# Optimization experiments

Measured on AMD Instinct MI355X. Metric: run time of the kernel, lower is better.

Reference implementation:

```python
import jax, jax.numpy as jnp
import numpy as np

B, T, F = 256, 512, 256
H, C = 1024, 128


def setup_inputs() -> dict:
    key = jax.random.key(0)
    ks = jax.random.split(key, 12)
    s = 0.05
    return {
        "y": jax.random.normal(ks[0], (B, T, F), jnp.float32),
        "W_ih1": jax.random.normal(ks[1], (4 * H, F), jnp.float32) * s,
        "W_hh1": jax.random.normal(ks[2], (4 * H, H), jnp.float32) * s,
        "b_ih1": jax.random.normal(ks[3], (4 * H,), jnp.float32) * s,
        "b_hh1": jax.random.normal(ks[4], (4 * H,), jnp.float32) * s,
        "W_ih2": jax.random.normal(ks[5], (4 * H, H), jnp.float32) * s,
        "W_hh2": jax.random.normal(ks[6], (4 * H, H), jnp.float32) * s,
        "b_ih2": jax.random.normal(ks[7], (4 * H,), jnp.float32) * s,
        "b_hh2": jax.random.normal(ks[8], (4 * H,), jnp.float32) * s,
        "W_out": jax.random.normal(ks[9], (C, H), jnp.float32) * s,
        "b_out": jax.random.normal(ks[10], (C,), jnp.float32) * s,
    }


def _lstm_cell(x, h, c, W_ih, W_hh, b_ih, b_hh):
    # PyTorch LSTMCell: gates ordered i, f, g, o
    gates = x @ W_ih.T + b_ih + h @ W_hh.T + b_hh
    i, f, g, o = jnp.split(gates, 4, axis=-1)
    i, f, o = jax.nn.sigmoid(i), jax.nn.sigmoid(f), jax.nn.sigmoid(o)
    g = jnp.tanh(g)
    c_new = f * c + i * g
    h_new = o * jnp.tanh(c_new)
    return h_new, c_new


def reference(y, W_ih1, W_hh1, b_ih1, b_hh1, W_ih2, W_hh2, b_ih2, b_hh2, W_out, b_out):
    n = y.shape[0]
    z = jnp.zeros((n, H), jnp.float32)

    def step(carry, x_t):
        h1, c1, h2, c2 = carry
        h1, c1 = _lstm_cell(x_t, h1, c1, W_ih1, W_hh1, b_ih1, b_hh1)
        h2, c2 = _lstm_cell(h1, h2, c2, W_ih2, W_hh2, b_ih2, b_hh2)
        h2 = jnp.tanh(h2)  # note: tanh'd h2 is also the recurrent state, as in source
        out = jax.nn.relu(h2 @ W_out.T + b_out)
        return (h1, c1, h2, c2), out

    xs = jnp.transpose(y, (1, 0, 2))  # [T, B, F]
    _, outs = jax.lax.scan(step, (z, z, z, z), xs)
    # return_sequences=False -> last timestep output [B, C]
    return outs[-1]
```

## Files before the change

### kernel.cpp

```cpp
#include <hip/hip_runtime.h>
#include <hip/hip_bf16.h>

#define Bb 256
#define Tt 512
#define Ff 256
#define Hh 1024
#define Cc 128
#define NBLK 256
#define NTHR 512

typedef __bf16 bf16;
typedef bf16 bf16x8 __attribute__((ext_vector_type(8)));
typedef float f32x4 __attribute__((ext_vector_type(4)));

#define MFMA(a, b, c) __builtin_amdgcn_mfma_f32_16x16x32_bf16(a, b, c, 0, 0, 0)

struct SMem {
    bf16x8 w[2 * 64 * 64];
    float scratch[32 * 129];
    float bias[32];
    bf16 hstage[8 * 256];
};

__device__ __forceinline__ float fsig(float x) {
    x = fminf(30.f, fmaxf(-30.f, x));
    return __builtin_amdgcn_rcpf(1.f + __expf(-x));
}
__device__ __forceinline__ float ftanh(float x) {
    x = fminf(15.f, fmaxf(-15.f, x));
    float e = __expf(2.f * x);
    return (e - 1.f) * __builtin_amdgcn_rcpf(e + 1.f);
}

#define STX4_SC1(p, v) \
    asm volatile("global_store_dwordx4 %0, %1, off sc1" :: "v"(p), "v"(v) : "memory")
#define LDX4_PLAIN(dst, base, OFF) \
    asm volatile("global_load_dwordx4 %0, %1, off offset:" #OFF : "=v"(dst) : "v"(base))

#define ISSUE_CHUNK(B0, B1, P0, P1) do { \
    LDX4_PLAIN(B0[0], (P0), 0);   LDX4_PLAIN(B0[1], (P0), 64);  LDX4_PLAIN(B0[2], (P0), 128); LDX4_PLAIN(B0[3], (P0), 192); \
    LDX4_PLAIN(B0[4], (P0), 256); LDX4_PLAIN(B0[5], (P0), 320); LDX4_PLAIN(B0[6], (P0), 384); LDX4_PLAIN(B0[7], (P0), 448); \
    LDX4_PLAIN(B1[0], (P1), 0);   LDX4_PLAIN(B1[1], (P1), 64);  LDX4_PLAIN(B1[2], (P1), 128); LDX4_PLAIN(B1[3], (P1), 192); \
    LDX4_PLAIN(B1[4], (P1), 256); LDX4_PLAIN(B1[5], (P1), 320); LDX4_PLAIN(B1[6], (P1), 384); LDX4_PLAIN(B1[7], (P1), 448); \
} while (0)

#define WAITV(N, B0, B1) \
    asm volatile("s_waitcnt vmcnt(" #N ")" : \
        "+v"(B0[0]), "+v"(B0[1]), "+v"(B0[2]), "+v"(B0[3]), \
        "+v"(B0[4]), "+v"(B0[5]), "+v"(B0[6]), "+v"(B0[7]), \
        "+v"(B1[0]), "+v"(B1[1]), "+v"(B1[2]), "+v"(B1[3]), \
        "+v"(B1[4]), "+v"(B1[5]), "+v"(B1[6]), "+v"(B1[7]) :: "memory")

#define MFMA8(ABASE, B0, B1) do { \
    _Pragma("unroll") \
    for (int _i = 0; _i < 8; ++_i) { \
        bf16x8 _a0 = wA0[((ABASE) + _i) * 64 + lane]; \
        bf16x8 _a1 = wA1[((ABASE) + _i) * 64 + lane]; \
        bf16x8 _b0 = __builtin_bit_cast(bf16x8, B0[_i]); \
        bf16x8 _b1 = __builtin_bit_cast(bf16x8, B1[_i]); \
        acc00 = MFMA(_a0, _b0, acc00); acc10 = MFMA(_a1, _b0, acc10); \
        acc01 = MFMA(_a0, _b1, acc01); acc11 = MFMA(_a1, _b1, acc11); \
    } \
} while (0)

__device__ __forceinline__ void mm32(const bf16x8* __restrict__ wA0, const bf16x8* __restrict__ wA1,
                                     int abase, const bf16* p0, const bf16* p1, int lane,
                                     f32x4& acc00, f32x4& acc01, f32x4& acc10, f32x4& acc11)
{
    f32x4 bx0[8], bx1[8], by0[8], by1[8];
    asm volatile("s_waitcnt vmcnt(0)" ::: "memory");
    ISSUE_CHUNK(bx0, bx1, p0, p1);
    ISSUE_CHUNK(by0, by1, p0 + 256, p1 + 256);
    WAITV(16, bx0, bx1);
    MFMA8(abase + 0, bx0, bx1);
    ISSUE_CHUNK(bx0, bx1, p0 + 512, p1 + 512);
    WAITV(16, by0, by1);
    MFMA8(abase + 8, by0, by1);
    ISSUE_CHUNK(by0, by1, p0 + 768, p1 + 768);
    WAITV(16, bx0, bx1);
    MFMA8(abase + 16, bx0, bx1);
    WAITV(0, by0, by1);
    MFMA8(abase + 24, by0, by1);
}

__device__ __forceinline__ void epilogue(SMem& sm, f32x4 acc00, f32x4 acc01, f32x4 acc10, f32x4 acc11,
                                         float creg[4], bf16* hdst, int hu0, bool extra_tanh) {
    const int tid = threadIdx.x;
    const int lane = tid & 63, wv = tid >> 6, quad = lane >> 4, l15 = lane & 15;
    const int colb = (wv & 3) * 32;
    #pragma unroll
    for (int ph = 0; ph < 2; ++ph) {
        if ((wv >> 2) == ph) {
            #pragma unroll
            for (int r = 0; r < 4; ++r) {
                sm.scratch[(quad * 4 + r) * 129 + colb + l15]           = acc00[r];
                sm.scratch[(quad * 4 + r) * 129 + colb + 16 + l15]      = acc01[r];
                sm.scratch[(16 + quad * 4 + r) * 129 + colb + l15]      = acc10[r];
                sm.scratch[(16 + quad * 4 + r) * 129 + colb + 16 + l15] = acc11[r];
            }
        }
        __syncthreads();
        #pragma unroll
        for (int pi = 0; pi < 2; ++pi) {
            int idx = pi * NTHR + tid;
            int bl = idx & 127, hu = idx >> 7;
            float gi = sm.scratch[hu * 129 + bl]        + sm.bias[hu];
            float gf = sm.scratch[(8 + hu) * 129 + bl]  + sm.bias[8 + hu];
            float gg = sm.scratch[(16 + hu) * 129 + bl] + sm.bias[16 + hu];
            float go = sm.scratch[(24 + hu) * 129 + bl] + sm.bias[24 + hu];
            float iv = fsig(gi), fv = fsig(gf), gv = ftanh(gg), ov = fsig(go);
            float c = fv * creg[ph * 2 + pi] + iv * gv;
            creg[ph * 2 + pi] = c;
            float h = ov * ftanh(c);
            if (extra_tanh) h = ftanh(h);
            sm.hstage[hu * 256 + (bl + 128 * ph)] = (bf16)h;
        }
        __syncthreads();
    }
    if (tid < 256) {
        bf16x8 v;
        #pragma unroll
        for (int e = 0; e < 8; ++e) v[e] = sm.hstage[e * 256 + tid];
        bf16* p = hdst + (size_t)tid * Hh + hu0;
        f32x4 pv = __builtin_bit_cast(f32x4, v);
        STX4_SC1(p, pv);
    }
}

__global__ void __launch_bounds__(NTHR, 2)
lstm_kernel(const float* __restrict__ y,
            const float* __restrict__ Wih1, const float* __restrict__ Whh1,
            const float* __restrict__ bih1, const float* __restrict__ bhh1,
            const float* __restrict__ Wih2, const float* __restrict__ Whh2,
            const float* __restrict__ bih2, const float* __restrict__ bhh2,
            const float* __restrict__ Wout, const float* __restrict__ bout,
            float* __restrict__ out,
            bf16* __restrict__ h1b0, bf16* __restrict__ h1b1,
            bf16* __restrict__ h2b0, bf16* __restrict__ h2b1,
            char* __restrict__ ctl)
{
    __shared__ SMem sm;
    const int tid = threadIdx.x;
    const int bid = blockIdx.x;
    const bool isL2 = bid >= 128;
    const int hu0 = (bid & 127) * 8;
    const int KI = isL2 ? 64 : 40;
    const int lane = tid & 63;
    const int wv = tid >> 6;
    const int quad = lane >> 4;
    const int l15 = lane & 15;

    unsigned* boot   = (unsigned*)ctl;
    unsigned* arrive = (unsigned*)(ctl + 2048);

    if (tid < 32) {
        int gate = tid >> 3, j = tid & 7;
        int grow = gate * Hh + hu0 + j;
        sm.bias[tid] = isL2 ? (bih2[grow] + bhh2[grow]) : (bih1[grow] + bhh1[grow]);
    }
    for (int slot = tid; slot < 2 * KI * 64; slot += NTHR) {
        int mt = slot / (KI * 64);
        int ki = (slot / 64) % KI;
        int ln = slot & 63;
        int row = mt * 16 + (ln & 15);
        int k = ki * 32 + (ln >> 4) * 8;
        int gate = row >> 3, j = row & 7;
        int grow = gate * Hh + hu0 + j;
        const float* src;
        if (!isL2) src = (k < Ff) ? (Wih1 + (size_t)grow * Ff + k) : (Whh1 + (size_t)grow * Hh + (k - Ff));
        else       src = (k < Hh) ? (Wih2 + (size_t)grow * Hh + k) : (Whh2 + (size_t)grow * Hh + (k - Hh));
        bf16x8 fr;
        #pragma unroll
        for (int e = 0; e < 8; ++e) fr[e] = (bf16)src[e];
        sm.w[slot] = fr;
    }
    float creg[4] = {0.f, 0.f, 0.f, 0.f};
    __syncthreads();

    if (tid == 0)
        __hip_atomic_store(&boot[bid], 1u, __ATOMIC_RELAXED, __HIP_MEMORY_SCOPE_AGENT);
    if (tid < 64) {
        for (;;) {
            int ok = 1;
            #pragma unroll
            for (int j = 0; j < 4; ++j)
                ok &= (__hip_atomic_load(&boot[tid * 4 + j], __ATOMIC_RELAXED,
                                         __HIP_MEMORY_SCOPE_AGENT) >= 1u);
            if (__all(ok)) break;
            __builtin_amdgcn_s_sleep(4);
        }
    }
    __syncthreads();

    const int nb0 = wv * 32 + l15;
    const bf16x8* wA0 = sm.w;
    const bf16x8* wA1 = sm.w + KI * 64;

    for (int s = 0; s <= Tt; ++s) {
        const int t = isL2 ? (s - 1) : s;
        const bool active = isL2 ? (s >= 1) : (s < Tt);
        f32x4 acc00 = {0,0,0,0}, acc01 = {0,0,0,0}, acc10 = {0,0,0,0}, acc11 = {0,0,0,0};

        if (!isL2 && active) {
            const f32x4* x0v = (const f32x4*)(y + ((size_t)nb0 * Tt + t) * Ff) + quad * 2;
            const f32x4* x1v = x0v + (size_t)16 * Tt * (Ff / 4);
            #pragma unroll
            for (int ki = 0; ki < 8; ++ki) {
                bf16x8 a0 = wA0[ki * 64 + lane];
                bf16x8 a1 = wA1[ki * 64 + lane];
                f32x4 u0 = x0v[ki * 8], u1 = x0v[ki * 8 + 1];
                f32x4 w0 = x1v[ki * 8], w1 = x1v[ki * 8 + 1];
                bf16x8 b0, b1;
                #pragma unroll
                for (int e = 0; e < 4; ++e) {
                    b0[e] = (bf16)u0[e]; b0[4 + e] = (bf16)u1[e];
                    b1[e] = (bf16)w0[e]; b1[4 + e] = (bf16)w1[e];
                }
                acc00 = MFMA(a0, b0, acc00); acc10 = MFMA(a1, b0, acc10);
                acc01 = MFMA(a0, b1, acc01); acc11 = MFMA(a1, b1, acc11);
            }
        }

        if (s >= 1) {
            const unsigned e = (unsigned)s;
            if (tid < 64) {
                for (;;) {
                    int ok = 1;
                    #pragma unroll
                    for (int j = 0; j < 4; ++j)
                        ok &= (__hip_atomic_load(&arrive[tid * 4 + j], __ATOMIC_RELAXED,
                                                 __HIP_MEMORY_SCOPE_AGENT) >= e);
                    if (__all(ok)) break;
                    __builtin_amdgcn_s_sleep(2);
                }
                __builtin_amdgcn_fence(__ATOMIC_ACQUIRE, "agent");
            }
            __syncthreads();
        }

        if (active) {
            const bf16* h1rd = ((s - 1) & 1) ? h1b1 : h1b0;
            if (!isL2) {
                if (t > 0) {
                    const bf16* p0 = h1rd + (size_t)nb0 * Hh + quad * 8;
                    mm32(wA0, wA1, 8, p0, p0 + 16 * Hh, lane, acc00, acc01, acc10, acc11);
                }
                epilogue(sm, acc00, acc01, acc10, acc11, creg, (t & 1) ? h1b1 : h1b0, hu0, false);
            } else {
                const bf16* p0 = h1rd + (size_t)nb0 * Hh + quad * 8;
                mm32(wA0, wA1, 0, p0, p0 + 16 * Hh, lane, acc00, acc01, acc10, acc11);
                if (t > 0) {
                    const bf16* h2rd = (s & 1) ? h2b1 : h2b0;
                    const bf16* q0 = h2rd + (size_t)nb0 * Hh + quad * 8;
                    mm32(wA0, wA1, 32, q0, q0 + 16 * Hh, lane, acc00, acc01, acc10, acc11);
                }
                epilogue(sm, acc00, acc01, acc10, acc11, creg, (t & 1) ? h2b1 : h2b0, hu0, true);
            }
        }

        __syncthreads();
        if (tid == 0)
            __hip_atomic_store(&arrive[bid], (unsigned)(s + 1), __ATOMIC_RELAXED,
                               __HIP_MEMORY_SCOPE_AGENT);
    }

    {
        const unsigned e = (unsigned)(Tt + 1);
        if (tid < 64) {
            for (;;) {
                int ok = 1;
                #pragma unroll
                for (int j = 0; j < 4; ++j)
                    ok &= (__hip_atomic_load(&arrive[tid * 4 + j], __ATOMIC_RELAXED,
                                             __HIP_MEMORY_SCOPE_AGENT) >= e);
                if (__all(ok)) break;
                __builtin_amdgcn_s_sleep(2);
            }
            __builtin_amdgcn_fence(__ATOMIC_ACQUIRE, "agent");
        }
        __syncthreads();
    }

    if (bid < 16) {
        const int bb = bid * 16 + l15;
        const float* ap = Wout + (size_t)(wv * 16 + l15) * Hh + quad * 8;
        const bf16* bp = h2b1 + (size_t)bb * Hh + quad * 8;
        f32x4 acc = {0,0,0,0};
        #pragma unroll 4
        for (int ki = 0; ki < 32; ++ki) {
            bf16x8 a;
            #pragma unroll
            for (int e = 0; e < 8; ++e) a[e] = (bf16)ap[ki * 32 + e];
            bf16x8 b = *(const bf16x8*)(bp + ki * 32);
            acc = MFMA(a, b, acc);
        }
        #pragma unroll
        for (int r = 0; r < 4; ++r) {
            int orow = wv * 16 + quad * 4 + r;
            float v = acc[r] + bout[orow];
            out[(size_t)bb * Cc + orow] = fmaxf(v, 0.f);
        }
    }
}

extern "C" void kernel_launch(void* const* d_in, const int* in_sizes, int n_in,
                              void* d_out, int out_size, void* d_ws, size_t ws_size,
                              hipStream_t stream) {
    const float* y    = (const float*)d_in[0];
    const float* Wih1 = (const float*)d_in[1];
    const float* Whh1 = (const float*)d_in[2];
    const float* bih1 = (const float*)d_in[3];
    const float* bhh1 = (const float*)d_in[4];
    const float* Wih2 = (const float*)d_in[5];
    const float* Whh2 = (const float*)d_in[6];
    const float* bih2 = (const float*)d_in[7];
    const float* bhh2 = (const float*)d_in[8];
    const float* Wout = (const float*)d_in[9];
    const float* bout = (const float*)d_in[10];
    float* out = (float*)d_out;

    char* wsteal = (char*)d_in[2] + ((size_t)4 * Hh * Hh * sizeof(float) - 4 * 524288);
    bf16* h1b0 = (bf16*)(wsteal);
    bf16* h1b1 = (bf16*)(wsteal + 1 * 524288);
    bf16* h2b0 = (bf16*)(wsteal + 2 * 524288);
    bf16* h2b1 = (bf16*)(wsteal + 3 * 524288);

    char* ctl = (char*)d_ws;
    hipMemsetAsync(ctl, 0, 32768, stream);

    void* args[] = { &y, &Wih1, &Whh1, &bih1, &bhh1, &Wih2, &Whh2, &bih2, &bhh2,
                     &Wout, &bout, &out, &h1b0, &h1b1, &h2b0, &h2b1, &ctl };
    hipLaunchCooperativeKernel((void*)lstm_kernel, dim3(NBLK), dim3(NTHR), args, 0, stream);
}
```

Measured before the change: 19.18 ms.

## Interleave gate rows so LSTM epilogue runs in registers; rotate K chunks per block

Weight rows are reordered so each MFMA output quad holds the i,f,g,o gates of one hidden unit for one batch row. The cell update can then be computed directly from accumulator registers, with biases held in registers. This removes the shared-memory scratch transpose and most of the block barriers in the per-step epilogue. The K-chunk load order is also rotated per block to spread simultaneous reads of the shared h buffers, and layer 2's two matmuls are merged into one pipelined 64-chunk loop. The trade-off is more address arithmetic and a different summation order, which slightly changes the rounding of the results.

```diff
diff --git a/kernel.cpp b/kernel.cpp
--- a/kernel.cpp
+++ b/kernel.cpp
@@ -17,9 +17,7 @@
 
 struct SMem {
     bf16x8 w[2 * 64 * 64];
-    float scratch[32 * 129];
-    float bias[32];
-    bf16 hstage[8 * 256];
+    bf16 hstage[256 * 8];
 };
 
 __device__ __forceinline__ float fsig(float x) {
@@ -63,64 +61,90 @@
     } \
 } while (0)
 
+__device__ __forceinline__ const bf16* phsel(int idx, const bf16* p, const bf16* q) {
+    return ((idx < 4) ? p : q) + (idx & 3) * 256;
+}
+
 __device__ __forceinline__ void mm32(const bf16x8* __restrict__ wA0, const bf16x8* __restrict__ wA1,
-                                     int abase, const bf16* p0, const bf16* p1, int lane,
+                                     int abase, const bf16* p0, const bf16* p1, int lane, int rot,
                                      f32x4& acc00, f32x4& acc01, f32x4& acc10, f32x4& acc11)
 {
     f32x4 bx0[8], bx1[8], by0[8], by1[8];
+    const int c0 = rot & 3, c1 = (rot + 1) & 3, c2 = (rot + 2) & 3, c3 = (rot + 3) & 3;
+    const bf16* a0 = p0 + c0 * 256; const bf16* a1 = p1 + c0 * 256;
+    const bf16* b0 = p0 + c1 * 256; const bf16* b1 = p1 + c1 * 256;
+    const bf16* d0 = p0 + c2 * 256; const bf16* d1 = p1 + c2 * 256;
+    const bf16* e0 = p0 + c3 * 256; const bf16* e1 = p1 + c3 * 256;
     asm volatile("s_waitcnt vmcnt(0)" ::: "memory");
-    ISSUE_CHUNK(bx0, bx1, p0, p1);
-    ISSUE_CHUNK(by0, by1, p0 + 256, p1 + 256);
+    ISSUE_CHUNK(bx0, bx1, a0, a1);
+    ISSUE_CHUNK(by0, by1, b0, b1);
     WAITV(16, bx0, bx1);
-    MFMA8(abase + 0, bx0, bx1);
-    ISSUE_CHUNK(bx0, bx1, p0 + 512, p1 + 512);
+    MFMA8(abase + c0 * 8, bx0, bx1);
+    ISSUE_CHUNK(bx0, bx1, d0, d1);
     WAITV(16, by0, by1);
-    MFMA8(abase + 8, by0, by1);
-    ISSUE_CHUNK(by0, by1, p0 + 768, p1 + 768);
+    MFMA8(abase + c1 * 8, by0, by1);
+    ISSUE_CHUNK(by0, by1, e0, e1);
     WAITV(16, bx0, bx1);
-    MFMA8(abase + 16, bx0, bx1);
+    MFMA8(abase + c2 * 8, bx0, bx1);
     WAITV(0, by0, by1);
-    MFMA8(abase + 24, by0, by1);
+    MFMA8(abase + c3 * 8, by0, by1);
+}
+
+__device__ __forceinline__ void mm64(const bf16x8* __restrict__ wA0, const bf16x8* __restrict__ wA1,
+                                     const bf16* p0, const bf16* p1,
+                                     const bf16* q0, const bf16* q1, int lane, int rot,
+                                     f32x4& acc00, f32x4& acc01, f32x4& acc10, f32x4& acc11)
+{
+    f32x4 bx0[8], bx1[8], by0[8], by1[8];
+    const int i0 = rot & 7, i1 = (rot + 1) & 7, i2 = (rot + 2) & 7, i3 = (rot + 3) & 7;
+    const int i4 = (rot + 4) & 7, i5 = (rot + 5) & 7, i6 = (rot + 6) & 7, i7 = (rot + 7) & 7;
+    asm volatile("s_waitcnt vmcnt(0)" ::: "memory");
+    { const bf16* u0 = phsel(i0, p0, q0); const bf16* u1 = phsel(i0, p1, q1); ISSUE_CHUNK(bx0, bx1, u0, u1); }
+    { const bf16* u0 = phsel(i1, p0, q0); const bf16* u1 = phsel(i1, p1, q1); ISSUE_CHUNK(by0, by1, u0, u1); }
+    WAITV(16, bx0, bx1); MFMA8(i0 * 8, bx0, bx1);
+    { const bf16* u0 = phsel(i2, p0, q0); const bf16* u1 = phsel(i2, p1, q1); ISSUE_CHUNK(bx0, bx1, u0, u1); }
+    WAITV(16, by0, by1); MFMA8(i1 * 8, by0, by1);
+    { const bf16* u0 = phsel(i3, p0, q0); const bf16* u1 = phsel(i3, p1, q1); ISSUE_CHUNK(by0, by1, u0, u1); }
+    WAITV(16, bx0, bx1); MFMA8(i2 * 8, bx0, bx1);
+    { const bf16* u0 = phsel(i4, p0, q0); const bf16* u1 = phsel(i4, p1, q1); ISSUE_CHUNK(bx0, bx1, u0, u1); }
+    WAITV(16, by0, by1); MFMA8(i3 * 8, by0, by1);
+    { const bf16* u0 = phsel(i5, p0, q0); const bf16* u1 = phsel(i5, p1, q1); ISSUE_CHUNK(by0, by1, u0, u1); }
+    WAITV(16, bx0, bx1); MFMA8(i4 * 8, bx0, bx1);
+    { const bf16* u0 = phsel(i6, p0, q0); const bf16* u1 = phsel(i6, p1, q1); ISSUE_CHUNK(bx0, bx1, u0, u1); }
+    WAITV(16, by0, by1); MFMA8(i5 * 8, by0, by1);
+    { const bf16* u0 = phsel(i7, p0, q0); const bf16* u1 = phsel(i7, p1, q1); ISSUE_CHUNK(by0, by1, u0, u1); }
+    WAITV(16, bx0, bx1); MFMA8(i6 * 8, bx0, bx1);
+    WAITV(0, by0, by1); MFMA8(i7 * 8, by0, by1);
+}
+
+__device__ __forceinline__ float lstm_cell(const f32x4& acc, const f32x4& bq, float& c, bool extra_tanh) {
+    float iv = fsig(acc[0] + bq[0]);
+    float fv = fsig(acc[1] + bq[1]);
+    float gv = ftanh(acc[2] + bq[2]);
+    float ov = fsig(acc[3] + bq[3]);
+    float cn = fv * c + iv * gv;
+    c = cn;
+    float h = ov * ftanh(cn);
+    return extra_tanh ? ftanh(h) : h;
 }
 
 __device__ __forceinline__ void epilogue(SMem& sm, f32x4 acc00, f32x4 acc01, f32x4 acc10, f32x4 acc11,
+                                         const f32x4& bq0, const f32x4& bq1,
                                          float creg[4], bf16* hdst, int hu0, bool extra_tanh) {
     const int tid = threadIdx.x;
     const int lane = tid & 63, wv = tid >> 6, quad = lane >> 4, l15 = lane & 15;
-    const int colb = (wv & 3) * 32;
-    #pragma unroll
-    for (int ph = 0; ph < 2; ++ph) {
-        if ((wv >> 2) == ph) {
-            #pragma unroll
-            for (int r = 0; r < 4; ++r) {
-                sm.scratch[(quad * 4 + r) * 129 + colb + l15]           = acc00[r];
-                sm.scratch[(quad * 4 + r) * 129 + colb + 16 + l15]      = acc01[r];
-                sm.scratch[(16 + quad * 4 + r) * 129 + colb + l15]      = acc10[r];
-                sm.scratch[(16 + quad * 4 + r) * 129 + colb + 16 + l15] = acc11[r];
-            }
-        }
-        __syncthreads();
-        #pragma unroll
-        for (int pi = 0; pi < 2; ++pi) {
-            int idx = pi * NTHR + tid;
-            int bl = idx & 127, hu = idx >> 7;
-            float gi = sm.scratch[hu * 129 + bl]        + sm.bias[hu];
-            float gf = sm.scratch[(8 + hu) * 129 + bl]  + sm.bias[8 + hu];
-            float gg = sm.scratch[(16 + hu) * 129 + bl] + sm.bias[16 + hu];
-            float go = sm.scratch[(24 + hu) * 129 + bl] + sm.bias[24 + hu];
-            float iv = fsig(gi), fv = fsig(gf), gv = ftanh(gg), ov = fsig(go);
-            float c = fv * creg[ph * 2 + pi] + iv * gv;
-            creg[ph * 2 + pi] = c;
-            float h = ov * ftanh(c);
-            if (extra_tanh) h = ftanh(h);
-            sm.hstage[hu * 256 + (bl + 128 * ph)] = (bf16)h;
-        }
-        __syncthreads();
-    }
+    const int b0 = wv * 32 + l15;
+    float h00 = lstm_cell(acc00, bq0, creg[0], extra_tanh);
+    float h01 = lstm_cell(acc01, bq0, creg[1], extra_tanh);
+    float h10 = lstm_cell(acc10, bq1, creg[2], extra_tanh);
+    float h11 = lstm_cell(acc11, bq1, creg[3], extra_tanh);
+    sm.hstage[b0 * 8 + quad]            = (bf16)h00;
+    sm.hstage[(b0 + 16) * 8 + quad]     = (bf16)h01;
+    sm.hstage[b0 * 8 + 4 + quad]        = (bf16)h10;
+    sm.hstage[(b0 + 16) * 8 + 4 + quad] = (bf16)h11;
+    __syncthreads();
     if (tid < 256) {
-        bf16x8 v;
-        #pragma unroll
-        for (int e = 0; e < 8; ++e) v[e] = sm.hstage[e * 256 + tid];
+        bf16x8 v = *(const bf16x8*)&sm.hstage[tid * 8];
         bf16* p = hdst + (size_t)tid * Hh + hu0;
         f32x4 pv = __builtin_bit_cast(f32x4, v);
         STX4_SC1(p, pv);
@@ -149,22 +173,28 @@
     const int wv = tid >> 6;
     const int quad = lane >> 4;
     const int l15 = lane & 15;
+    const int rot4 = bid & 3;
+    const int rot8 = bid & 7;
 
     unsigned* boot   = (unsigned*)ctl;
     unsigned* arrive = (unsigned*)(ctl + 2048);
 
-    if (tid < 32) {
-        int gate = tid >> 3, j = tid & 7;
-        int grow = gate * Hh + hu0 + j;
-        sm.bias[tid] = isL2 ? (bih2[grow] + bhh2[grow]) : (bih1[grow] + bhh1[grow]);
+    f32x4 bq0, bq1;
+    #pragma unroll
+    for (int r = 0; r < 4; ++r) {
+        int g0 = r * Hh + hu0 + quad;
+        int g1 = r * Hh + hu0 + 4 + quad;
+        bq0[r] = isL2 ? (bih2[g0] + bhh2[g0]) : (bih1[g0] + bhh1[g0]);
+        bq1[r] = isL2 ? (bih2[g1] + bhh2[g1]) : (bih1[g1] + bhh1[g1]);
     }
     for (int slot = tid; slot < 2 * KI * 64; slot += NTHR) {
         int mt = slot / (KI * 64);
         int ki = (slot / 64) % KI;
         int ln = slot & 63;
-        int row = mt * 16 + (ln & 15);
+        int local = ln & 15;
         int k = ki * 32 + (ln >> 4) * 8;
-        int gate = row >> 3, j = row & 7;
+        int gate = local & 3;
+        int j = mt * 4 + (local >> 2);
         int grow = gate * Hh + hu0 + j;
         const float* src;
         if (!isL2) src = (k < Ff) ? (Wih1 + (size_t)grow * Ff + k) : (Whh1 + (size_t)grow * Hh + (k - Ff));
@@ -243,18 +273,22 @@
             if (!isL2) {
                 if (t > 0) {
                     const bf16* p0 = h1rd + (size_t)nb0 * Hh + quad * 8;
-                    mm32(wA0, wA1, 8, p0, p0 + 16 * Hh, lane, acc00, acc01, acc10, acc11);
+                    mm32(wA0, wA1, 8, p0, p0 + 16 * Hh, lane, rot4, acc00, acc01, acc10, acc11);
                 }
-                epilogue(sm, acc00, acc01, acc10, acc11, creg, (t & 1) ? h1b1 : h1b0, hu0, false);
+                epilogue(sm, acc00, acc01, acc10, acc11, bq0, bq1, creg,
+                         (t & 1) ? h1b1 : h1b0, hu0, false);
             } else {
                 const bf16* p0 = h1rd + (size_t)nb0 * Hh + quad * 8;
-                mm32(wA0, wA1, 0, p0, p0 + 16 * Hh, lane, acc00, acc01, acc10, acc11);
                 if (t > 0) {
                     const bf16* h2rd = (s & 1) ? h2b1 : h2b0;
                     const bf16* q0 = h2rd + (size_t)nb0 * Hh + quad * 8;
-                    mm32(wA0, wA1, 32, q0, q0 + 16 * Hh, lane, acc00, acc01, acc10, acc11);
+                    mm64(wA0, wA1, p0, p0 + 16 * Hh, q0, q0 + 16 * Hh, lane, rot8,
+                         acc00, acc01, acc10, acc11);
+                } else {
+                    mm32(wA0, wA1, 0, p0, p0 + 16 * Hh, lane, rot4, acc00, acc01, acc10, acc11);
                 }
-                epilogue(sm, acc00, acc01, acc10, acc11, creg, (t & 1) ? h2b1 : h2b0, hu0, true);
+                epilogue(sm, acc00, acc01, acc10, acc11, bq0, bq1, creg,
+                         (t & 1) ? h2b1 : h2b0, hu0, true);
             }
         }
 
```

New measurement: 18.56 ms. -3.2%, faster.
